# Kernel tuning notes

Measured on AMD Instinct MI355X. Metric: run time of the kernel, lower is better.

## Reference

```python
import jax, jax.numpy as jnp
import numpy as np

N = 5000        # nodes
F = 7699        # node feature dim (fixed by code)
E = 40000       # edges
ED = 3          # edge_dim (fixed by code)
H1, C1 = 4, 1024
H2, C2 = 1, 1024
NUM_OUT = 128
NEG_SLOPE = 0.2


def _glorot(key, shape):
    fan_in = shape[0]
    return jax.random.normal(key, shape, jnp.float32) / np.float32(np.sqrt(fan_in))


def setup_inputs() -> dict:
    key = jax.random.key(0)
    ks = jax.random.split(key, 16)
    x = jax.random.normal(ks[0], (N, F), jnp.float32)
    src = jax.random.randint(ks[1], (E,), 0, N)
    dst = jax.random.randint(ks[2], (E,), 0, N)
    src = jnp.where(src == dst, (src + 1) % N, src)  # no pre-existing self loops
    edge_index = jnp.stack([src, dst]).astype(jnp.int32)
    edge_attr = jax.random.normal(ks[3], (E, ED), jnp.float32)
    inp = {
        "x": x, "edge_index": edge_index, "edge_attr": edge_attr,
        # GATv2Conv #1: 7699 -> 1024, heads=4, edge_dim=3
        "W1l": _glorot(ks[4], (F, H1 * C1)), "b1l": jnp.zeros((H1 * C1,), jnp.float32),
        "W1r": _glorot(ks[5], (F, H1 * C1)), "b1r": jnp.zeros((H1 * C1,), jnp.float32),
        "W1e": _glorot(ks[6], (ED, H1 * C1)),
        "att1": _glorot(ks[7], (H1, C1)),
        "bias1": jnp.zeros((H1 * C1,), jnp.float32),
        # GATv2Conv #2: 4096 -> 1024, heads=1, edge_dim=3
        "W2l": _glorot(ks[8], (H1 * C1, H2 * C2)), "b2l": jnp.zeros((H2 * C2,), jnp.float32),
        "W2r": _glorot(ks[9], (H1 * C1, H2 * C2)), "b2r": jnp.zeros((H2 * C2,), jnp.float32),
        "W2e": _glorot(ks[10], (ED, H2 * C2)),
        "att2": _glorot(ks[11], (H2, C2)),
        "bias2": jnp.zeros((H2 * C2,), jnp.float32),
        # final Linear(1024, num_outputs)
        "Wlin": _glorot(ks[12], (C2, NUM_OUT)), "blin": jnp.zeros((NUM_OUT,), jnp.float32),
    }
    return inp


def gatv2_layer(x, src, dst, edge_attr, Wl, bl, Wr, br, We, att, bias, heads, out_ch):
    """PyG GATv2Conv with add_self_loops=True, fill_value='mean', concat=True."""
    n = x.shape[0]
    # self-loop edge_attr = mean of incoming edge attrs per node (fill_value='mean')
    deg = jax.ops.segment_sum(jnp.ones((src.shape[0],), jnp.float32), dst, num_segments=n)
    loop_attr = jax.ops.segment_sum(edge_attr, dst, num_segments=n) / jnp.maximum(deg, 1.0)[:, None]
    idx = jnp.arange(n, dtype=src.dtype)
    srcf = jnp.concatenate([src, idx])
    dstf = jnp.concatenate([dst, idx])
    ea = jnp.concatenate([edge_attr, loop_attr], axis=0)
    xl = (x @ Wl + bl).reshape(n, heads, out_ch)   # lin_l (source)
    xr = (x @ Wr + br).reshape(n, heads, out_ch)   # lin_r (target)
    ee = (ea @ We).reshape(-1, heads, out_ch)       # lin_edge (no bias)
    e = jax.nn.leaky_relu(xl[srcf] + xr[dstf] + ee, NEG_SLOPE)  # [E', H, C]
    logit = jnp.einsum('ehc,hc->eh', e, att)                     # [E', H]
    # segment softmax over destination nodes (every node has a self loop)
    m = jax.lax.stop_gradient(jax.ops.segment_max(logit, dstf, num_segments=n))
    a = jnp.exp(logit - m[dstf])
    denom = jax.ops.segment_sum(a, dstf, num_segments=n)
    alpha = a / (denom[dstf] + 1e-16)
    out = jax.ops.segment_sum(alpha[:, :, None] * xl[srcf], dstf, num_segments=n)  # [N,H,C]
    return out.reshape(n, heads * out_ch) + bias


def reference(x, edge_index, edge_attr,
              W1l, b1l, W1r, b1r, W1e, att1, bias1,
              W2l, b2l, W2r, b2r, W2e, att2, bias2,
              Wlin, blin):
    src, dst = edge_index[0], edge_index[1]
    h = gatv2_layer(x, src, dst, edge_attr, W1l, b1l, W1r, b1r, W1e, att1, bias1, H1, C1)
    h = gatv2_layer(h, src, dst, edge_attr, W2l, b2l, W2r, b2r, W2e, att2, bias2, H2, C2)
    return h @ Wlin + blin
```

## Files before the change

kernel.cpp:

```cpp
#include <hip/hip_runtime.h>
#include <cstdint>
#include <cstddef>

#define N_NODES 5000
#define F_IN    7699
#define KP1     7712
#define KT1     241
#define MP      5120
#define E_EDGES 40000
#define EFULL   45000
#define HC1     4096
#define N1      8192
#define HC2     1024
#define N2      2048
#define NOUT    128
#define GM128   (MP / 128)

typedef __bf16 bf16x8 __attribute__((ext_vector_type(8)));
typedef float  f32x4  __attribute__((ext_vector_type(4)));
typedef float  f32x16 __attribute__((ext_vector_type(16)));
typedef unsigned short u16x8 __attribute__((ext_vector_type(8)));
typedef _Float16 f16;
typedef _Float16 f16x8 __attribute__((ext_vector_type(8)));

using as1_uchar = unsigned char __attribute__((address_space(1)));
using as3_uchar = unsigned char __attribute__((address_space(3)));

__device__ __forceinline__ unsigned short f2bf(float f) {
  union { float f; unsigned int u; } v; v.f = f;
  return (unsigned short)((v.u + 0x7fffu + ((v.u >> 16) & 1u)) >> 16);
}
__device__ __forceinline__ float bf2f(unsigned short h) {
  union { unsigned int u; float f; } v; v.u = ((unsigned int)h) << 16;
  return v.f;
}

__device__ __forceinline__ void gload16(const void* g, void* l) {
  __builtin_amdgcn_global_load_lds(
      reinterpret_cast<const as1_uchar*>(reinterpret_cast<uintptr_t>(g)),
      reinterpret_cast<as3_uchar*>(reinterpret_cast<uintptr_t>(l)),
      16, 0, 0);
}



__global__ void k_split_x(const float* __restrict__ x, unsigned short* __restrict__ hi,
                          unsigned short* __restrict__ lo) {
  const int C8 = KP1 / 8;
  int ci = blockIdx.x * 256 + threadIdx.x;
  if (ci >= MP * C8) return;
  int r = ci / C8, c8 = ci % C8;
  int c = c8 * 8;
  u16x8 hb, lb;
  #pragma unroll
  for (int j = 0; j < 8; ++j) {
    float v = 0.f;
    if (r < N_NODES && (c + j) < F_IN) v = x[(size_t)r * F_IN + c + j];
    unsigned short h = f2bf(v);
    hb[j] = h; lb[j] = f2bf(v - bf2f(h));
  }
  size_t off = ((size_t)((r >> 7) * KT1 + (c >> 5)) * 4 + ((c >> 3) & 3)) * 1024 + (r & 127) * 8;
  *(u16x8*)&hi[off] = hb;
  *(u16x8*)&lo[off] = lb;
}


__global__ void k_split_w(const float* __restrict__ W,
                          unsigned short* __restrict__ hi, unsigned short* __restrict__ lo,
                          int K, int Nsrc, int c0, int KT, int rowOffset) {
  __shared__ float tile[32][33];
  const int tid = threadIdx.x;
  const int kt = blockIdx.x;
  const int n0 = blockIdx.y * 32;
  #pragma unroll
  for (int i = tid >> 5; i < 32; i += 8) {
    int k = kt * 32 + i;
    tile[i][tid & 31] = (k < K) ? W[(size_t)k * Nsrc + c0 + n0 + (tid & 31)] : 0.f;
  }
  __syncthreads();
  if (tid < 128) {
    const int nn = tid >> 2, kc = (tid & 3) << 3;
    const int n = rowOffset + n0 + nn;
    u16x8 hb, lb;
    #pragma unroll
    for (int j = 0; j < 8; ++j) {
      float v = tile[kc + j][nn];
      unsigned short h = f2bf(v);
      hb[j] = h; lb[j] = f2bf(v - bf2f(h));
    }
    size_t off = ((size_t)((n >> 7) * KT + kt) * 4 + (kc >> 3)) * 1024 + (n & 127) * 8;
    *(u16x8*)&hi[off] = hb;
    *(u16x8*)&lo[off] = lb;
  }
}


template <int OF16>
__global__ __launch_bounds__(256, 2) void k_gemm_bb(
    const unsigned short* __restrict__ Ahi, const unsigned short* __restrict__ Alo,
    const unsigned short* __restrict__ Bhi, const unsigned short* __restrict__ Blo,
    void* __restrict__ Cp, const float* __restrict__ bias0, const float* __restrict__ bias1,
    int halfN, int M, int Nc, int ldC, int KT32, int nbn)
{
  __shared__ __align__(16) unsigned short S[4 * 8192];

  const int tid = threadIdx.x;
  const int lane = tid & 63;
  const int w = tid >> 6;
  const int wm = w >> 1, wn = w & 1;

  const int nwg = gridDim.x;
  const int qq = nwg >> 3, rr = nwg & 7;
  const int xcd = blockIdx.x & 7, idx = blockIdx.x >> 3;
  const int wg = (xcd < rr ? xcd * (qq + 1) : rr * (qq + 1) + (xcd - rr) * qq) + idx;
  const int bm = wg / nbn, bn = wg % nbn;

  f32x16 acc[2][2] = {};

  const unsigned short* gbase = (w == 0) ? Ahi : (w == 1) ? Alo : (w == 2) ? Bhi : Blo;
  const int brow = (w < 2) ? bm : bn;
  const unsigned short* gsrc[4];
  int dd[4];
  #pragma unroll
  for (int s = 0; s < 4; ++s) {
    const int p = s >> 1, hf = s & 1;
    gsrc[s] = gbase + (size_t)brow * KT32 * 4096 + p * 1024 + hf * 512 + lane * 8;
    dd[s] = w * 2048 + p * 1024 + hf * 512;
  }

  auto stage = [&](int kt16, int bufo) {
    const size_t o = (size_t)kt16 * 2048;
    #pragma unroll
    for (int s = 0; s < 4; ++s) gload16(gsrc[s] + o, &S[bufo + dd[s]]);
  };

  const int r5 = lane & 31, h5 = lane >> 5;
  int ra[2], cb[2];
  #pragma unroll
  for (int i = 0; i < 2; ++i) ra[i] = h5 * 1024 + (wm * 64 + i * 32 + r5) * 8;
  #pragma unroll
  for (int j = 0; j < 2; ++j) cb[j] = 4096 + h5 * 1024 + (wn * 64 + j * 32 + r5) * 8;

  struct Frags { bf16x8 ah[2], al[2], bh[2], bl[2]; };
  auto rdfr = [&](Frags& f, int bufo) {
    #pragma unroll
    for (int i = 0; i < 2; ++i) {
      f.ah[i] = *(const bf16x8*)&S[bufo + ra[i]];
      f.al[i] = *(const bf16x8*)&S[bufo + 2048 + ra[i]];
    }
    #pragma unroll
    for (int j = 0; j < 2; ++j) {
      f.bh[j] = *(const bf16x8*)&S[bufo + cb[j]];
      f.bl[j] = *(const bf16x8*)&S[bufo + 2048 + cb[j]];
    }
  };
  auto domfma = [&](Frags& f) {
    __builtin_amdgcn_s_setprio(1);
    #pragma unroll
    for (int j = 0; j < 2; ++j)
      #pragma unroll
      for (int i = 0; i < 2; ++i) {
        acc[i][j] = __builtin_amdgcn_mfma_f32_32x32x16_bf16(f.ah[i], f.bh[j], acc[i][j], 0, 0, 0);
        acc[i][j] = __builtin_amdgcn_mfma_f32_32x32x16_bf16(f.al[i], f.bh[j], acc[i][j], 0, 0, 0);
        acc[i][j] = __builtin_amdgcn_mfma_f32_32x32x16_bf16(f.ah[i], f.bl[j], acc[i][j], 0, 0, 0);
      }
    __builtin_amdgcn_s_setprio(0);
  };

  const int KT16 = KT32 * 2;

  stage(0, 0);
  stage(1, 8192);
  stage(2, 16384);
  asm volatile("s_waitcnt vmcnt(4)" ::: "memory");
  __builtin_amdgcn_s_barrier();
  Frags fA, fB;
  rdfr(fA, 0);

  int o0 = 0, o1 = 8192, o2 = 16384, o3 = 24576;
  for (int kt = 0; kt < KT16; kt += 2) {
    stage((kt + 3 < KT16) ? kt + 3 : KT16 - 1, o3);
    rdfr(fB, o1);
    domfma(fA);
    asm volatile("s_waitcnt vmcnt(4)" ::: "memory");
    __builtin_amdgcn_s_barrier();
    stage((kt + 4 < KT16) ? kt + 4 : KT16 - 1, o0);
    rdfr(fA, o2);
    domfma(fB);
    asm volatile("s_waitcnt vmcnt(4)" ::: "memory");
    __builtin_amdgcn_s_barrier();
    int t0 = o0, t1 = o1;
    o0 = o2; o1 = o3; o2 = t0; o3 = t1;
  }

  #pragma unroll
  for (int i = 0; i < 2; ++i) {
    #pragma unroll
    for (int j = 0; j < 2; ++j) {
      const int gc = bn * 128 + wn * 64 + j * 32 + r5;
      if (gc < Nc) {
        const float bv = (gc < halfN) ? bias0[gc] : bias1[gc - halfN];
        #pragma unroll
        for (int reg = 0; reg < 16; ++reg) {
          const int gr = bm * 128 + wm * 64 + i * 32 + (reg & 3) + 8 * (reg >> 2) + 4 * h5;
          if (gr < M) {
            float v = acc[i][j][reg] + bv;
            if (OF16) ((f16*)Cp)[(size_t)gr * ldC + gc] = (f16)v;
            else      ((float*)Cp)[(size_t)gr * ldC + gc] = v;
          }
        }
      }
    }
  }
}


__global__ void k_deg(const int* __restrict__ dst, const float* __restrict__ ea,
                      float* __restrict__ deg, float* __restrict__ lattr, int E) {
  int e = blockIdx.x * 256 + threadIdx.x;
  if (e >= E) return;
  int d = dst[e];
  atomicAdd(&deg[d], 1.f);
  atomicAdd(&lattr[d * 3 + 0], ea[e * 3 + 0]);
  atomicAdd(&lattr[d * 3 + 1], ea[e * 3 + 1]);
  atomicAdd(&lattr[d * 3 + 2], ea[e * 3 + 2]);
}

__global__ void k_lattr_fin(float* __restrict__ lattr, const float* __restrict__ deg, int n) {
  int i = blockIdx.x * 256 + threadIdx.x;
  if (i >= n) return;
  float dv = fmaxf(deg[i], 1.f);
  lattr[i * 3 + 0] /= dv; lattr[i * 3 + 1] /= dv; lattr[i * 3 + 2] /= dv;
}

__global__ void k_eafull(const float* __restrict__ ea, const float* __restrict__ lattr,
                         float* __restrict__ eaf, int E, int n) {
  int e = blockIdx.x * 256 + threadIdx.x;
  if (e >= E + n) return;
  const float* s = (e < E) ? &ea[(size_t)e * 3] : &lattr[(size_t)(e - E) * 3];
  eaf[e * 3 + 0] = s[0]; eaf[e * 3 + 1] = s[1]; eaf[e * 3 + 2] = s[2];
}

__global__ void k_count(const int* __restrict__ dst, int* __restrict__ cnt, int E, int n) {
  int e = blockIdx.x * 256 + threadIdx.x;
  if (e >= E + n) return;
  int d = (e < E) ? dst[e] : (e - E);
  atomicAdd(&cnt[d], 1);
}

__global__ void k_scan(const int* __restrict__ cnt, int* __restrict__ rowptr, int n) {
  int lane = threadIdx.x;
  int run = 0;
  for (int base = 0; base < n; base += 64) {
    int i = base + lane;
    int v = (i < n) ? cnt[i] : 0;
    #pragma unroll
    for (int off = 1; off < 64; off <<= 1) {
      int t = __shfl_up(v, off, 64);
      if (lane >= off) v += t;
    }
    if (i < n) rowptr[i + 1] = run + v;
    run += __shfl(v, 63, 64);
  }
  if (lane == 0) rowptr[0] = 0;
}

__global__ void k_fill(const int* __restrict__ dst, const int* __restrict__ rowptr,
                       int* __restrict__ fillc, int* __restrict__ elist, int E, int n) {
  int e = blockIdx.x * 256 + threadIdx.x;
  if (e >= E + n) return;
  int d = (e < E) ? dst[e] : (e - E);
  int pos = rowptr[d] + atomicAdd(&fillc[d], 1);
  elist[pos] = e;
}


template <int H, int ITERS>
__global__ __launch_bounds__(256) void k_logit(
    const f16* __restrict__ xl, const f16* __restrict__ xr, int strideX,
    const float* __restrict__ eaf, const float* __restrict__ We, const float* __restrict__ att,
    const int* __restrict__ src, const int* __restrict__ dst, int E,
    float* __restrict__ logit)
{
  const int e = blockIdx.x;
  const int tid = threadIdx.x;
  int s, d;
  if (e < E) { s = src[e]; d = dst[e]; } else { s = e - E; d = s; }
  const float ea0 = eaf[e * 3 + 0], ea1 = eaf[e * 3 + 1], ea2 = eaf[e * 3 + 2];
  constexpr int HC = ITERS * 256;
  const f16* rl = xl + (size_t)s * strideX;
  const f16* rr = xr + (size_t)d * strideX;
  float acc[H];
  #pragma unroll
  for (int h = 0; h < H; ++h) acc[h] = 0.f;
  #pragma unroll
  for (int i = 0; i < ITERS; ++i) {
    int hc = tid + (i << 8);
    float v = (float)rl[hc] + (float)rr[hc]
            + ea0 * We[hc] + ea1 * We[HC + hc] + ea2 * We[2 * HC + hc];
    v = (v > 0.f) ? v : 0.2f * v;
    acc[i >> 2] += v * att[hc];
  }
  __shared__ float red[H][4];
  const int lane = tid & 63, wv = tid >> 6;
  #pragma unroll
  for (int h = 0; h < H; ++h) {
    float v = acc[h];
    #pragma unroll
    for (int off = 32; off > 0; off >>= 1) v += __shfl_down(v, off, 64);
    if (lane == 0) red[h][wv] = v;
  }
  __syncthreads();
  if (tid < H)
    logit[(size_t)e * H + tid] = red[tid][0] + red[tid][1] + red[tid][2] + red[tid][3];
}

template <int H>
__global__ void k_stats(const float* __restrict__ logit, const int* __restrict__ rowptr,
                        const int* __restrict__ elist, float* __restrict__ mb, float* __restrict__ db)
{
  const int n = blockIdx.x;
  const int lane = threadIdx.x;
  const int start = rowptr[n], end = rowptr[n + 1];
  #pragma unroll
  for (int h = 0; h < H; ++h) {
    float m = -1e30f;
    for (int p = start + lane; p < end; p += 64)
      m = fmaxf(m, logit[(size_t)elist[p] * H + h]);
    #pragma unroll
    for (int off = 32; off > 0; off >>= 1) m = fmaxf(m, __shfl_down(m, off, 64));
    m = __shfl(m, 0, 64);
    float sum = 0.f;
    for (int p = start + lane; p < end; p += 64)
      sum += __expf(logit[(size_t)elist[p] * H + h] - m);
    #pragma unroll
    for (int off = 32; off > 0; off >>= 1) sum += __shfl_down(sum, off, 64);
    if (lane == 0) { mb[n * H + h] = m; db[n * H + h] = sum; }
  }
}

template <int H, int NC8, int KTo>
__global__ __launch_bounds__(256) void k_agg(
    const f16* __restrict__ xl, int strideX,
    const int* __restrict__ rowptr, const int* __restrict__ elist, const int* __restrict__ src,
    const float* __restrict__ logit, const float* __restrict__ mb, const float* __restrict__ db,
    const float* __restrict__ bias,
    unsigned short* __restrict__ ohi, unsigned short* __restrict__ olo, int E)
{
  const int n = blockIdx.x;
  const int tid = threadIdx.x;
  constexpr int HC = H * 1024;
  float acc[NC8][8];
  #pragma unroll
  for (int q = 0; q < NC8; ++q)
    #pragma unroll
    for (int j = 0; j < 8; ++j) acc[q][j] = 0.f;
  const int start = rowptr[n], end = rowptr[n + 1];
  float mloc[H], dloc[H];
  #pragma unroll
  for (int h = 0; h < H; ++h) { mloc[h] = mb[n * H + h]; dloc[h] = db[n * H + h] + 1e-16f; }
  for (int p = start; p < end; ++p) {
    const int e = elist[p];
    const int s = (e < E) ? src[e] : (e - E);
    float al[H];
    #pragma unroll
    for (int h = 0; h < H; ++h)
      al[h] = __expf(logit[(size_t)e * H + h] - mloc[h]) / dloc[h];
    const f16* row = xl + (size_t)s * strideX;
    #pragma unroll
    for (int q = 0; q < NC8; ++q) {
      const int c8 = tid + q * 256;
      if (c8 * 8 < HC) {
        float a = (H == 4) ? ((tid & 128) ? al[2 * q + 1] : al[2 * q]) : al[0];
        f16x8 v = *(const f16x8*)(row + c8 * 8);
        #pragma unroll
        for (int j = 0; j < 8; ++j) acc[q][j] += a * (float)v[j];
      }
    }
  }
  #pragma unroll
  for (int q = 0; q < NC8; ++q) {
    const int c8 = tid + q * 256;
    if (c8 * 8 < HC) {
      u16x8 hb, lb;
      #pragma unroll
      for (int j = 0; j < 8; ++j) {
        float v = acc[q][j] + bias[c8 * 8 + j];
        unsigned short h = f2bf(v);
        hb[j] = h; lb[j] = f2bf(v - bf2f(h));
      }
      size_t off = ((size_t)((n >> 7) * KTo + (c8 >> 2)) * 4 + (c8 & 3)) * 1024 + (n & 127) * 8;
      *(u16x8*)&ohi[off] = hb;
      *(u16x8*)&olo[off] = lb;
    }
  }
}


extern "C" void kernel_launch(void* const* d_in, const int* in_sizes, int n_in,
                              void* d_out, int out_size, void* d_ws, size_t ws_size,
                              hipStream_t stream) {
  const float* x    = (const float*)d_in[0];
  const int*   eidx = (const int*)d_in[1];
  const float* eattr= (const float*)d_in[2];
  const float* W1l  = (const float*)d_in[3];
  const float* b1l  = (const float*)d_in[4];
  const float* W1r  = (const float*)d_in[5];
  const float* b1r  = (const float*)d_in[6];
  const float* W1e  = (const float*)d_in[7];
  const float* att1 = (const float*)d_in[8];
  const float* bias1= (const float*)d_in[9];
  const float* W2l  = (const float*)d_in[10];
  const float* b2l  = (const float*)d_in[11];
  const float* W2r  = (const float*)d_in[12];
  const float* b2r  = (const float*)d_in[13];
  const float* W2e  = (const float*)d_in[14];
  const float* att2 = (const float*)d_in[15];
  const float* bias2= (const float*)d_in[16];
  const float* Wlin = (const float*)d_in[17];
  const float* blin = (const float*)d_in[18];
  float* out = (float*)d_out;

  char* ws = (char*)d_ws;
  const int* srcp = eidx;
  const int* dstp = eidx + E_EDGES;

  auto alignup = [](size_t v) { return (v + 255) & ~(size_t)255; };

  size_t mo = 0;
  auto take = [&](size_t sz) { size_t r = mo; mo = alignup(mo + sz); return r; };
  const size_t oLATTR = take((size_t)N_NODES * 3 * 4);
  const size_t oDEG   = take((size_t)N_NODES * 4);
  const size_t oEAF   = take((size_t)EFULL * 3 * 4);
  const size_t oCNT   = take((size_t)N_NODES * 4);
  const size_t oROW   = take((size_t)(N_NODES + 1) * 4);
  const size_t oFILL  = take((size_t)N_NODES * 4);
  const size_t oELIST = take((size_t)EFULL * 4);
  const size_t oLOGIT = take((size_t)EFULL * 4 * 4);
  const size_t oMB    = take((size_t)N_NODES * 4 * 4);
  const size_t oDB    = take((size_t)N_NODES * 4 * 4);
  const size_t oXHI   = take((size_t)MP * KP1 * 2);
  const size_t oXLO   = take((size_t)MP * KP1 * 2);
  const size_t oXLR   = take((size_t)N_NODES * N1 * 2);
  const size_t oBH    = take((size_t)N1 * KP1 * 2);
  const size_t oBL    = take((size_t)N1 * KP1 * 2);
  if (ws_size < mo) return;

  const size_t oH1HI = oXHI;
  const size_t oH1LO = oXLO;
  const size_t oXLR2 = oXLR;
  const size_t oH2HI = oXLR + 32ull * 1024 * 1024;
  const size_t oH2LO = oXLR + 48ull * 1024 * 1024;
  const size_t oB2H  = oBH;
  const size_t oB2L  = oBH + 32ull * 1024 * 1024;
  const size_t oB3H  = oBH;
  const size_t oB3L  = oBH + 1ull * 1024 * 1024;

  unsigned short* XHI  = (unsigned short*)(ws + oXHI);
  unsigned short* XLO  = (unsigned short*)(ws + oXLO);
  f16*            XLR  = (f16*)(ws + oXLR);
  unsigned short* BH   = (unsigned short*)(ws + oBH);
  unsigned short* BL   = (unsigned short*)(ws + oBL);
  float*          LATTR= (float*)(ws + oLATTR);
  float*          DEG  = (float*)(ws + oDEG);
  float*          EAF  = (float*)(ws + oEAF);
  int*            CNT  = (int*)(ws + oCNT);
  int*            ROWP = (int*)(ws + oROW);
  int*            FILLC= (int*)(ws + oFILL);
  int*            ELIST= (int*)(ws + oELIST);
  float*          LOGIT= (float*)(ws + oLOGIT);
  float*          MB   = (float*)(ws + oMB);
  float*          DB   = (float*)(ws + oDB);
  unsigned short* H1HI = (unsigned short*)(ws + oH1HI);
  unsigned short* H1LO = (unsigned short*)(ws + oH1LO);
  f16*            XLR2 = (f16*)(ws + oXLR2);
  unsigned short* H2HI = (unsigned short*)(ws + oH2HI);
  unsigned short* H2LO = (unsigned short*)(ws + oH2LO);
  unsigned short* B2H  = (unsigned short*)(ws + oB2H);
  unsigned short* B2L  = (unsigned short*)(ws + oB2L);
  unsigned short* B3H  = (unsigned short*)(ws + oB3H);
  unsigned short* B3L  = (unsigned short*)(ws + oB3L);

  hipMemsetAsync(ws + oDEG,   0, (size_t)N_NODES * 4, stream);
  hipMemsetAsync(ws + oLATTR, 0, (size_t)N_NODES * 3 * 4, stream);
  hipMemsetAsync(ws + oCNT,   0, (size_t)N_NODES * 4, stream);
  hipMemsetAsync(ws + oFILL,  0, (size_t)N_NODES * 4, stream);

  const int gE  = (E_EDGES + 255) / 256;
  const int gEF = (EFULL + 255) / 256;
  const int gN  = (N_NODES + 255) / 256;

  k_deg<<<gE, 256, 0, stream>>>(dstp, eattr, DEG, LATTR, E_EDGES);
  k_lattr_fin<<<gN, 256, 0, stream>>>(LATTR, DEG, N_NODES);
  k_eafull<<<gEF, 256, 0, stream>>>(eattr, LATTR, EAF, E_EDGES, N_NODES);
  k_count<<<gEF, 256, 0, stream>>>(dstp, CNT, E_EDGES, N_NODES);
  k_scan<<<1, 64, 0, stream>>>(CNT, ROWP, N_NODES);
  k_fill<<<gEF, 256, 0, stream>>>(dstp, ROWP, FILLC, ELIST, E_EDGES, N_NODES);

  k_split_x<<<MP * (KP1 / 8) / 256, 256, 0, stream>>>(x, XHI, XLO);
  k_split_w<<<dim3(KT1, HC1 / 32), 256, 0, stream>>>(W1l, BH, BL, F_IN, HC1, 0, KT1, 0);
  k_split_w<<<dim3(KT1, HC1 / 32), 256, 0, stream>>>(W1r, BH, BL, F_IN, HC1, 0, KT1, HC1);
  k_gemm_bb<1><<<GM128 * (N1 / 128), 256, 0, stream>>>(
      XHI, XLO, BH, BL, XLR, b1l, b1r, HC1, N_NODES, N1, N1, KT1, N1 / 128);

  k_logit<4, 16><<<EFULL, 256, 0, stream>>>(XLR, XLR + HC1, N1, EAF, W1e, att1, srcp, dstp, E_EDGES, LOGIT);
  k_stats<4><<<N_NODES, 64, 0, stream>>>(LOGIT, ROWP, ELIST, MB, DB);
  hipMemsetAsync(ws + oH1HI, 0, (size_t)MP * HC1 * 2, stream);
  hipMemsetAsync(ws + oH1LO, 0, (size_t)MP * HC1 * 2, stream);
  k_agg<4, 2, HC1 / 32><<<N_NODES, 256, 0, stream>>>(
      XLR, N1, ROWP, ELIST, srcp, LOGIT, MB, DB, bias1, H1HI, H1LO, E_EDGES);

  k_split_w<<<dim3(HC1 / 32, HC2 / 32), 256, 0, stream>>>(W2l, B2H, B2L, HC1, HC2, 0, HC1 / 32, 0);
  k_split_w<<<dim3(HC1 / 32, HC2 / 32), 256, 0, stream>>>(W2r, B2H, B2L, HC1, HC2, 0, HC1 / 32, HC2);
  k_gemm_bb<1><<<GM128 * (N2 / 128), 256, 0, stream>>>(
      H1HI, H1LO, B2H, B2L, XLR2, b2l, b2r, HC2, N_NODES, N2, N2, HC1 / 32, N2 / 128);

  k_logit<1, 4><<<EFULL, 256, 0, stream>>>(XLR2, XLR2 + HC2, N2, EAF, W2e, att2, srcp, dstp, E_EDGES, LOGIT);
  k_stats<1><<<N_NODES, 64, 0, stream>>>(LOGIT, ROWP, ELIST, MB, DB);
  hipMemsetAsync(ws + oH2HI, 0, (size_t)MP * HC2 * 2, stream);
  hipMemsetAsync(ws + oH2LO, 0, (size_t)MP * HC2 * 2, stream);
  k_agg<1, 1, HC2 / 32><<<N_NODES, 256, 0, stream>>>(
      XLR2, N2, ROWP, ELIST, srcp, LOGIT, MB, DB, bias2, H2HI, H2LO, E_EDGES);

  k_split_w<<<dim3(HC2 / 32, NOUT / 32), 256, 0, stream>>>(Wlin, B3H, B3L, HC2, NOUT, 0, HC2 / 32, 0);
  k_gemm_bb<0><<<GM128 * 1, 256, 0, stream>>>(
      H2HI, H2LO, B3H, B3L, out, blin, blin, NOUT, N_NODES, NOUT, NOUT, HC2 / 32, 1);
}
```

Measured before the change: 2.787 ms.

## Use 256-row GEMM tile for layer-1 projection and fuse logit with softmax stats

Adds a 512-thread GEMM kernel with 256x128 tiles and a 4-stage LDS pipeline for the large first-layer projection, doubling A-tile rows per block so each B tile is loaded half as often. It also replaces the per-edge logit kernel and the separate stats kernel with one per-destination-node kernel. That kernel keeps the xr row and edge weights in registers and computes an online max and sum for the softmax. The fused kernel walks edges serially with two barriers per edge, which may lose parallelism on high-degree nodes. The larger GEMM tile raises LDS and register pressure.

```diff
diff --git a/kernel.cpp b/kernel.cpp
--- a/kernel.cpp
+++ b/kernel.cpp
@@ -14,6 +14,7 @@
 #define HC2     1024
 #define N2      2048
 #define NOUT    128
+#define GM256   (MP / 256)
 #define GM128   (MP / 128)
 
 typedef __bf16 bf16x8 __attribute__((ext_vector_type(8)));
@@ -91,6 +92,135 @@
     size_t off = ((size_t)((n >> 7) * KT + kt) * 4 + (kc >> 3)) * 1024 + (n & 127) * 8;
     *(u16x8*)&hi[off] = hb;
     *(u16x8*)&lo[off] = lb;
+  }
+}
+
+
+template <int OF16>
+__global__ __launch_bounds__(512, 2) void k_gemm_big(
+    const unsigned short* __restrict__ Ahi, const unsigned short* __restrict__ Alo,
+    const unsigned short* __restrict__ Bhi, const unsigned short* __restrict__ Blo,
+    void* __restrict__ Cp, const float* __restrict__ bias0, const float* __restrict__ bias1,
+    int halfN, int M, int Nc, int ldC, int KT32, int nbn)
+{
+  __shared__ __align__(16) unsigned short S[4 * 12288];
+
+  const int tid = threadIdx.x;
+  const int lane = tid & 63;
+  const int w = tid >> 6;
+  const int wm = w >> 1, wn = w & 1;
+
+  const int nwg = gridDim.x;
+  const int qq = nwg >> 3, rr = nwg & 7;
+  const int xcd = blockIdx.x & 7, idx = blockIdx.x >> 3;
+  const int wg = (xcd < rr ? xcd * (qq + 1) : rr * (qq + 1) + (xcd - rr) * qq) + idx;
+  const int bm = wg / nbn, bn = wg % nbn;
+
+  f32x16 acc[2][2] = {};
+
+  const unsigned short* gsrc[3];
+  int dd[3];
+  #pragma unroll
+  for (int s = 0; s < 3; ++s) {
+    const int q = w * 3 + s;
+    const unsigned short* base; int dOff; size_t rowoff; int p, hf;
+    if (q < 8)       { int r_ = q;      base = Ahi; int t = r_ >> 2; p = (r_ >> 1) & 1; hf = r_ & 1;
+                       dOff = t * 2048 + p * 1024 + hf * 512; rowoff = (size_t)(bm * 2 + t) * KT32 * 4096; }
+    else if (q < 16) { int r_ = q - 8;  base = Alo; int t = r_ >> 2; p = (r_ >> 1) & 1; hf = r_ & 1;
+                       dOff = 4096 + t * 2048 + p * 1024 + hf * 512; rowoff = (size_t)(bm * 2 + t) * KT32 * 4096; }
+    else if (q < 20) { int r_ = q - 16; base = Bhi; p = (r_ >> 1) & 1; hf = r_ & 1;
+                       dOff = 8192 + p * 1024 + hf * 512; rowoff = (size_t)bn * KT32 * 4096; }
+    else             { int r_ = q - 20; base = Blo; p = (r_ >> 1) & 1; hf = r_ & 1;
+                       dOff = 10240 + p * 1024 + hf * 512; rowoff = (size_t)bn * KT32 * 4096; }
+    gsrc[s] = base + rowoff + p * 1024 + hf * 512 + lane * 8;
+    dd[s] = dOff;
+  }
+
+  auto stage = [&](int kt16, int bufo) {
+    const size_t o = (size_t)kt16 * 2048;
+    #pragma unroll
+    for (int s = 0; s < 3; ++s) gload16(gsrc[s] + o, &S[bufo + dd[s]]);
+  };
+
+  const int r5 = lane & 31, h5 = lane >> 5;
+  const int tA = wm >> 1;
+  const int rrA = (wm & 1) * 64;
+  int ra[2], cb[2];
+  #pragma unroll
+  for (int i = 0; i < 2; ++i) ra[i] = tA * 2048 + h5 * 1024 + (rrA + i * 32 + r5) * 8;
+  #pragma unroll
+  for (int j = 0; j < 2; ++j) cb[j] = 8192 + h5 * 1024 + (wn * 64 + j * 32 + r5) * 8;
+
+  struct Frags { bf16x8 ah[2], al[2], bh[2], bl[2]; };
+  auto rdfr = [&](Frags& f, int bufo) {
+    #pragma unroll
+    for (int i = 0; i < 2; ++i) {
+      f.ah[i] = *(const bf16x8*)&S[bufo + ra[i]];
+      f.al[i] = *(const bf16x8*)&S[bufo + 4096 + ra[i]];
+    }
+    #pragma unroll
+    for (int j = 0; j < 2; ++j) {
+      f.bh[j] = *(const bf16x8*)&S[bufo + cb[j]];
+      f.bl[j] = *(const bf16x8*)&S[bufo + 2048 + cb[j]];
+    }
+  };
+  auto domfma = [&](Frags& f) {
+    __builtin_amdgcn_s_setprio(1);
+    #pragma unroll
+    for (int j = 0; j < 2; ++j)
+      #pragma unroll
+      for (int i = 0; i < 2; ++i) {
+        acc[i][j] = __builtin_amdgcn_mfma_f32_32x32x16_bf16(f.ah[i], f.bh[j], acc[i][j], 0, 0, 0);
+        acc[i][j] = __builtin_amdgcn_mfma_f32_32x32x16_bf16(f.al[i], f.bh[j], acc[i][j], 0, 0, 0);
+        acc[i][j] = __builtin_amdgcn_mfma_f32_32x32x16_bf16(f.ah[i], f.bl[j], acc[i][j], 0, 0, 0);
+      }
+    __builtin_amdgcn_s_setprio(0);
+  };
+
+  const int KT16 = KT32 * 2;
+
+  stage(0, 0);
+  stage(1, 12288);
+  stage(2, 24576);
+  asm volatile("s_waitcnt vmcnt(3)" ::: "memory");
+  __builtin_amdgcn_s_barrier();
+  Frags fA, fB;
+  rdfr(fA, 0);
+
+  int o0 = 0, o1 = 12288, o2 = 24576, o3 = 36864;
+  for (int kt = 0; kt < KT16; kt += 2) {
+    stage((kt + 3 < KT16) ? kt + 3 : KT16 - 1, o3);
+    rdfr(fB, o1);
+    domfma(fA);
+    asm volatile("s_waitcnt vmcnt(3)" ::: "memory");
+    __builtin_amdgcn_s_barrier();
+    stage((kt + 4 < KT16) ? kt + 4 : KT16 - 1, o0);
+    rdfr(fA, o2);
+    domfma(fB);
+    asm volatile("s_waitcnt vmcnt(3)" ::: "memory");
+    __builtin_amdgcn_s_barrier();
+    int t0 = o0, t1 = o1;
+    o0 = o2; o1 = o3; o2 = t0; o3 = t1;
+  }
+
+  #pragma unroll
+  for (int i = 0; i < 2; ++i) {
+    #pragma unroll
+    for (int j = 0; j < 2; ++j) {
+      const int gc = bn * 128 + wn * 64 + j * 32 + r5;
+      if (gc < Nc) {
+        const float bv = (gc < halfN) ? bias0[gc] : bias1[gc - halfN];
+        #pragma unroll
+        for (int reg = 0; reg < 16; ++reg) {
+          const int gr = bm * 256 + wm * 64 + i * 32 + (reg & 3) + 8 * (reg >> 2) + 4 * h5;
+          if (gr < M) {
+            float v = acc[i][j][reg] + bv;
+            if (OF16) ((f16*)Cp)[(size_t)gr * ldC + gc] = (f16)v;
+            else      ((float*)Cp)[(size_t)gr * ldC + gc] = v;
+          }
+        }
+      }
+    }
   }
 }
 
@@ -276,67 +406,62 @@
 
 
 template <int H, int ITERS>
-__global__ __launch_bounds__(256) void k_logit(
+__global__ __launch_bounds__(256) void k_logit_stats(
     const f16* __restrict__ xl, const f16* __restrict__ xr, int strideX,
     const float* __restrict__ eaf, const float* __restrict__ We, const float* __restrict__ att,
-    const int* __restrict__ src, const int* __restrict__ dst, int E,
-    float* __restrict__ logit)
+    const int* __restrict__ rowptr, const int* __restrict__ elist, const int* __restrict__ src,
+    int E, float* __restrict__ logit, float* __restrict__ mb, float* __restrict__ db)
 {
-  const int e = blockIdx.x;
+  const int n = blockIdx.x;
   const int tid = threadIdx.x;
-  int s, d;
-  if (e < E) { s = src[e]; d = dst[e]; } else { s = e - E; d = s; }
-  const float ea0 = eaf[e * 3 + 0], ea1 = eaf[e * 3 + 1], ea2 = eaf[e * 3 + 2];
   constexpr int HC = ITERS * 256;
-  const f16* rl = xl + (size_t)s * strideX;
-  const f16* rr = xr + (size_t)d * strideX;
-  float acc[H];
-  #pragma unroll
-  for (int h = 0; h < H; ++h) acc[h] = 0.f;
+  float xrv[ITERS], w0[ITERS], w1[ITERS], w2[ITERS], av[ITERS];
+  const f16* rr = xr + (size_t)n * strideX;
   #pragma unroll
   for (int i = 0; i < ITERS; ++i) {
-    int hc = tid + (i << 8);
-    float v = (float)rl[hc] + (float)rr[hc]
-            + ea0 * We[hc] + ea1 * We[HC + hc] + ea2 * We[2 * HC + hc];
-    v = (v > 0.f) ? v : 0.2f * v;
-    acc[i >> 2] += v * att[hc];
-  }
+    const int hc = tid + (i << 8);
+    xrv[i] = (float)rr[hc];
+    w0[i] = We[hc]; w1[i] = We[HC + hc]; w2[i] = We[2 * HC + hc];
+    av[i] = att[hc];
+  }
+  const int start = rowptr[n], end = rowptr[n + 1];
   __shared__ float red[H][4];
   const int lane = tid & 63, wv = tid >> 6;
-  #pragma unroll
-  for (int h = 0; h < H; ++h) {
-    float v = acc[h];
-    #pragma unroll
-    for (int off = 32; off > 0; off >>= 1) v += __shfl_down(v, off, 64);
-    if (lane == 0) red[h][wv] = v;
-  }
-  __syncthreads();
-  if (tid < H)
-    logit[(size_t)e * H + tid] = red[tid][0] + red[tid][1] + red[tid][2] + red[tid][3];
-}
-
-template <int H>
-__global__ void k_stats(const float* __restrict__ logit, const int* __restrict__ rowptr,
-                        const int* __restrict__ elist, float* __restrict__ mb, float* __restrict__ db)
-{
-  const int n = blockIdx.x;
-  const int lane = threadIdx.x;
-  const int start = rowptr[n], end = rowptr[n + 1];
-  #pragma unroll
-  for (int h = 0; h < H; ++h) {
-    float m = -1e30f;
-    for (int p = start + lane; p < end; p += 64)
-      m = fmaxf(m, logit[(size_t)elist[p] * H + h]);
-    #pragma unroll
-    for (int off = 32; off > 0; off >>= 1) m = fmaxf(m, __shfl_down(m, off, 64));
-    m = __shfl(m, 0, 64);
-    float sum = 0.f;
-    for (int p = start + lane; p < end; p += 64)
-      sum += __expf(logit[(size_t)elist[p] * H + h] - m);
-    #pragma unroll
-    for (int off = 32; off > 0; off >>= 1) sum += __shfl_down(sum, off, 64);
-    if (lane == 0) { mb[n * H + h] = m; db[n * H + h] = sum; }
-  }
+  float mh = -1e30f, sh = 0.f;
+
+  for (int p = start; p < end; ++p) {
+    const int e = elist[p];
+    const int s = (e < E) ? src[e] : (e - E);
+    const float ea0 = eaf[e * 3 + 0], ea1 = eaf[e * 3 + 1], ea2 = eaf[e * 3 + 2];
+    const f16* rl = xl + (size_t)s * strideX;
+    float acc[H];
+    #pragma unroll
+    for (int h = 0; h < H; ++h) acc[h] = 0.f;
+    #pragma unroll
+    for (int i = 0; i < ITERS; ++i) {
+      const int hc = tid + (i << 8);
+      float v = (float)rl[hc] + xrv[i] + ea0 * w0[i] + ea1 * w1[i] + ea2 * w2[i];
+      v = (v > 0.f) ? v : 0.2f * v;
+      acc[i >> 2] += v * av[i];
+    }
+    #pragma unroll
+    for (int h = 0; h < H; ++h) {
+      float v = acc[h];
+      #pragma unroll
+      for (int off = 32; off > 0; off >>= 1) v += __shfl_down(v, off, 64);
+      if (lane == 0) red[h][wv] = v;
+    }
+    __syncthreads();
+    if (tid < H) {
+      const float l = red[tid][0] + red[tid][1] + red[tid][2] + red[tid][3];
+      logit[(size_t)e * H + tid] = l;
+      const float mn = fmaxf(mh, l);
+      sh = sh * __expf(mh - mn) + __expf(l - mn);
+      mh = mn;
+    }
+    __syncthreads();
+  }
+  if (tid < H) { mb[n * H + tid] = mh; db[n * H + tid] = sh; }
 }
 
 template <int H, int NC8, int KTo>
@@ -500,11 +625,11 @@
   k_split_x<<<MP * (KP1 / 8) / 256, 256, 0, stream>>>(x, XHI, XLO);
   k_split_w<<<dim3(KT1, HC1 / 32), 256, 0, stream>>>(W1l, BH, BL, F_IN, HC1, 0, KT1, 0);
   k_split_w<<<dim3(KT1, HC1 / 32), 256, 0, stream>>>(W1r, BH, BL, F_IN, HC1, 0, KT1, HC1);
-  k_gemm_bb<1><<<GM128 * (N1 / 128), 256, 0, stream>>>(
+  k_gemm_big<1><<<GM256 * (N1 / 128), 512, 0, stream>>>(
       XHI, XLO, BH, BL, XLR, b1l, b1r, HC1, N_NODES, N1, N1, KT1, N1 / 128);
 
-  k_logit<4, 16><<<EFULL, 256, 0, stream>>>(XLR, XLR + HC1, N1, EAF, W1e, att1, srcp, dstp, E_EDGES, LOGIT);
-  k_stats<4><<<N_NODES, 64, 0, stream>>>(LOGIT, ROWP, ELIST, MB, DB);
+  k_logit_stats<4, 16><<<N_NODES, 256, 0, stream>>>(
+      XLR, XLR + HC1, N1, EAF, W1e, att1, ROWP, ELIST, srcp, E_EDGES, LOGIT, MB, DB);
   hipMemsetAsync(ws + oH1HI, 0, (size_t)MP * HC1 * 2, stream);
   hipMemsetAsync(ws + oH1LO, 0, (size_t)MP * HC1 * 2, stream);
   k_agg<4, 2, HC1 / 32><<<N_NODES, 256, 0, stream>>>(
@@ -515,8 +640,8 @@
   k_gemm_bb<1><<<GM128 * (N2 / 128), 256, 0, stream>>>(
       H1HI, H1LO, B2H, B2L, XLR2, b2l, b2r, HC2, N_NODES, N2, N2, HC1 / 32, N2 / 128);
 
-  k_logit<1, 4><<<EFULL, 256, 0, stream>>>(XLR2, XLR2 + HC2, N2, EAF, W2e, att2, srcp, dstp, E_EDGES, LOGIT);
-  k_stats<1><<<N_NODES, 64, 0, stream>>>(LOGIT, ROWP, ELIST, MB, DB);
+  k_logit_stats<1, 4><<<N_NODES, 256, 0, stream>>>(
+      XLR2, XLR2 + HC2, N2, EAF, W2e, att2, ROWP, ELIST, srcp, E_EDGES, LOGIT, MB, DB);
   hipMemsetAsync(ws + oH2HI, 0, (size_t)MP * HC2 * 2, stream);
   hipMemsetAsync(ws + oH2LO, 0, (size_t)MP * HC2 * 2, stream);
   k_agg<1, 1, HC2 / 32><<<N_NODES, 256, 0, stream>>>(
```

Result: faster. 2.660 ms (-4.6%).
